# Kernel optimization log

Measured on AMD Instinct MI355X. Metric: run time of the kernel, lower is better.

The kernel has to match this reference:

```python
import jax, jax.numpy as jnp
import numpy as np

D_MODEL = 1024
N_HEADS = 16
HEAD_DIM = D_MODEL // N_HEADS


def setup_inputs() -> dict:
    key = jax.random.key(0)
    kx, kq, kk, kv, ko = jax.random.split(key, 5)
    B, S = 4, 2048
    scale = 0.02
    return {
        "x": jax.random.normal(kx, (B, S, D_MODEL), dtype=jnp.float32),
        "Wq": jax.random.normal(kq, (D_MODEL, D_MODEL), dtype=jnp.float32) * scale,
        "Wk": jax.random.normal(kk, (D_MODEL, HEAD_DIM), dtype=jnp.float32) * scale,
        "Wv": jax.random.normal(kv, (D_MODEL, HEAD_DIM), dtype=jnp.float32) * scale,
        "Wo": jax.random.normal(ko, (D_MODEL, D_MODEL), dtype=jnp.float32) * scale,
    }


def reference(x, Wq, Wk, Wv, Wo):
    B, S, _ = x.shape
    # Q: [B, H, S, hd]; K, V: [B, S, hd] shared across heads (MQA)
    Q = (x @ Wq).reshape(B, S, N_HEADS, HEAD_DIM).transpose(0, 2, 1, 3)
    K = x @ Wk
    V = x @ Wv
    # scores: [B, H, S, S]
    scores = jnp.einsum("bhqd,bkd->bhqk", Q, K) / jnp.sqrt(jnp.float32(HEAD_DIM))
    attn = jax.nn.softmax(scores, axis=-1)
    out = jnp.einsum("bhqk,bkd->bhqd", attn, V)  # [B, H, S, hd]
    out = out.transpose(0, 2, 1, 3).reshape(B, S, D_MODEL)
    return out @ Wo
```

## Files before the change

kernel.cpp:

```cpp
#include <hip/hip_runtime.h>
#include <hip/hip_bf16.h>

typedef __bf16  bf16x8  __attribute__((ext_vector_type(8)));
typedef __bf16  bf16x4  __attribute__((ext_vector_type(4)));
typedef float   f32x4   __attribute__((ext_vector_type(4)));
typedef unsigned short ushort8 __attribute__((ext_vector_type(8)));

#define D_MODEL 1024
#define HEAD_DIM 64
#define N_HEADS 16
#define BATCH 4
#define SEQ 2048
#define ROWS (BATCH*SEQ)
#define QKV_LD 1152
#define VT_LD 2080

#define AS1 __attribute__((address_space(1)))
#define AS3 __attribute__((address_space(3)))

static __device__ inline float exp2_fast(float x) {
  float r; asm("v_exp_f32 %0, %1" : "=v"(r) : "v"(x)); return r;
}

__global__ __launch_bounds__(256) void k_f32_to_bf16(const float* __restrict__ in,
                                                     __bf16* __restrict__ out, int n) {
  int i = (blockIdx.x * 256 + threadIdx.x) * 8;
  if (i >= n) return;
  float4 a = *(const float4*)(in + i);
  float4 b = *(const float4*)(in + i + 4);
  __bf16 r[8] __attribute__((aligned(16))) =
      {(__bf16)a.x,(__bf16)a.y,(__bf16)a.z,(__bf16)a.w,
       (__bf16)b.x,(__bf16)b.y,(__bf16)b.z,(__bf16)b.w};
  *(ushort8*)(out + i) = *(const ushort8*)r;
}

__global__ __launch_bounds__(256) void k_transpose_f32_bf16(const float* __restrict__ in,
                                                            __bf16* __restrict__ out,
                                                            int R, int C, float scale) {
  __shared__ float t[32][33];
  int tx = threadIdx.x & 31, ty = threadIdx.x >> 5;
  int r0 = blockIdx.y * 32, c0 = blockIdx.x * 32;
  #pragma unroll
  for (int i = 0; i < 4; ++i)
    t[ty + i*8][tx] = in[(size_t)(r0 + ty + i*8) * C + c0 + tx];
  __syncthreads();
  #pragma unroll
  for (int i = 0; i < 4; ++i)
    out[(size_t)(c0 + ty + i*8) * R + r0 + tx] = (__bf16)(t[tx][ty + i*8] * scale);
}

template<typename OUT_T>
__global__ __launch_bounds__(256) void k_gemm(const __bf16* __restrict__ A,
                                              const __bf16* __restrict__ Bt,
                                              OUT_T* __restrict__ C,
                                              int M, int N, int K) {
  __shared__ __bf16 As[2][128*32] __attribute__((aligned(16)));
  __shared__ __bf16 Bs[2][128*32] __attribute__((aligned(16)));
  const int tid  = threadIdx.x;
  const int lane = tid & 63, wave = tid >> 6;
  const int wm = wave >> 1, wn = wave & 1;
  const int l15 = lane & 15, lhi = lane >> 4;
  const int arow0 = blockIdx.x * 128;
  const int brow0 = blockIdx.y * 128;
  f32x4 acc[4][4] = {};
  const int srow = lane >> 2;
  const int scol = (lane & 3) * 8;
  const int nt = K >> 5;

  auto stage = [&](int t, int buf) {
    #pragma unroll
    for (int i = 0; i < 2; ++i) {
      int chunk = i*4 + wave;
      int r = chunk*16 + srow;
      __builtin_amdgcn_global_load_lds(
          (const AS1 unsigned int*)(A  + (size_t)(arow0 + r)*K + t*32 + scol),
          (AS3 unsigned int*)(&As[buf][0] + chunk*512), 16, 0, 0);
      __builtin_amdgcn_global_load_lds(
          (const AS1 unsigned int*)(Bt + (size_t)(brow0 + r)*K + t*32 + scol),
          (AS3 unsigned int*)(&Bs[buf][0] + chunk*512), 16, 0, 0);
    }
  };

  stage(0, 0);
  asm volatile("s_waitcnt vmcnt(0)" ::: "memory");
  __builtin_amdgcn_s_barrier();

  for (int t = 0; t < nt; ++t) {
    const int cur = t & 1;
    if (t + 1 < nt) stage(t + 1, cur ^ 1);
    bf16x8 af[4], bfr[4];
    #pragma unroll
    for (int m = 0; m < 4; ++m)
      af[m] = *(const bf16x8*)(&As[cur][0] + (wm*64 + m*16 + l15)*32 + lhi*8);
    #pragma unroll
    for (int n = 0; n < 4; ++n)
      bfr[n] = *(const bf16x8*)(&Bs[cur][0] + (wn*64 + n*16 + l15)*32 + lhi*8);
    #pragma unroll
    for (int m = 0; m < 4; ++m)
      #pragma unroll
      for (int n = 0; n < 4; ++n)
        acc[m][n] = __builtin_amdgcn_mfma_f32_16x16x32_bf16(af[m], bfr[n], acc[m][n], 0, 0, 0);
    asm volatile("s_waitcnt vmcnt(0)" ::: "memory");
    __builtin_amdgcn_s_barrier();
  }
  #pragma unroll
  for (int m = 0; m < 4; ++m)
    #pragma unroll
    for (int n = 0; n < 4; ++n) {
      int row = arow0 + wm*64 + m*16 + lhi*4;
      int col = brow0 + wn*64 + n*16 + l15;
      #pragma unroll
      for (int r = 0; r < 4; ++r)
        C[(size_t)(row + r) * N + col] = (OUT_T)acc[m][n][r];
    }
}

__global__ __launch_bounds__(256) void k_vt_split(const __bf16* __restrict__ QKV,
                                                  __bf16* __restrict__ Vt) {
  __shared__ __bf16 t[64][72] __attribute__((aligned(16)));
  int st = blockIdx.x, b = blockIdx.y;
  int tid = threadIdx.x;
  int rr = tid >> 3, cc = (tid & 7) * 8;
  #pragma unroll
  for (int i = 0; i < 2; ++i) {
    int s = rr + i*32;
    *(ushort8*)&t[s][cc] =
      *(const ushort8*)(QKV + (size_t)(b*SEQ + st*64 + s) * QKV_LD + 1088 + cc);
  }
  __syncthreads();
  #pragma unroll
  for (int i = 0; i < 2; ++i) {
    int d = rr + i*32;
    __bf16 tmp[8] __attribute__((aligned(16)));
    #pragma unroll
    for (int j = 0; j < 8; ++j) tmp[j] = t[cc + j][d];
    *(ushort8*)(Vt + (size_t)(b*64 + d) * VT_LD + st*64 + cc) = *(const ushort8*)tmp;
  }
}

__global__ __launch_bounds__(512, 4) void k_attn(const __bf16* __restrict__ QKV,
                                                 const __bf16* __restrict__ Vt,
                                                 __bf16* __restrict__ O) {
  __shared__ __bf16 Kl[2][64*64];
  __shared__ __bf16 Vl[2][64*64];
  __shared__ __bf16 Pl[8][32*64];
  const int qt = blockIdx.x, h = blockIdx.y, b = blockIdx.z;
  const int tid = threadIdx.x, lane = tid & 63, w = tid >> 6;
  const int l15 = lane & 15, lhi = lane >> 4;
  const int l7 = l15 & 7;

  const int srow = lane >> 3;
  const int j8   = lane & 7;
  const int row_t = w*8 + srow;
  const int jsrc = j8 ^ srow;
  const __bf16* Kg = QKV + (size_t)b*SEQ*QKV_LD + 1024;
  const __bf16* Vg = Vt  + (size_t)b*64*VT_LD;

  auto stage = [&](int t, int buf) {
    __builtin_amdgcn_global_load_lds(
        (const AS1 unsigned int*)(Kg + (size_t)(t*64 + row_t)*QKV_LD + jsrc*8),
        (AS3 unsigned int*)(&Kl[buf][0] + w*512), 16, 0, 0);
    __builtin_amdgcn_global_load_lds(
        (const AS1 unsigned int*)(Vg + (size_t)row_t*VT_LD + t*64 + jsrc*8),
        (AS3 unsigned int*)(&Vl[buf][0] + w*512), 16, 0, 0);
  };

  stage(0, 0);

  bf16x8 aq[2][2];
  {
    const __bf16* qp = QKV + (size_t)(b*SEQ + qt*256 + w*32 + l15)*QKV_LD + h*HEAD_DIM;
    aq[0][0] = *(const bf16x8*)(qp +               lhi*8);
    aq[0][1] = *(const bf16x8*)(qp +          32 + lhi*8);
    aq[1][0] = *(const bf16x8*)(qp + 16*QKV_LD +      lhi*8);
    aq[1][1] = *(const bf16x8*)(qp + 16*QKV_LD + 32 + lhi*8);
  }

  f32x4 oacc[2][4] = {};
  float mrun[2] = {-__builtin_inff(), -__builtin_inff()};
  float lrun[2] = {0.f, 0.f};

  asm volatile("s_waitcnt vmcnt(0)" ::: "memory");
  __builtin_amdgcn_s_barrier();

  for (int t = 0; t < SEQ/64; ++t) {
    const int cur = t & 1;
    if (t < SEQ/64 - 1) {
      stage(t+1, cur^1);
      asm volatile("s_waitcnt vmcnt(2)" ::: "memory");
    } else {
      asm volatile("s_waitcnt vmcnt(0)" ::: "memory");
    }
    const char* Kc = (const char*)&Kl[cur][0];
    const char* Vc = (const char*)&Vl[cur][0];

    f32x4 s[2][4] = {};
    __builtin_amdgcn_s_setprio(1);
    #pragma unroll
    for (int n = 0; n < 4; ++n) {
      const int key = n*16 + l15;
      bf16x8 kb0 = *(const bf16x8*)(Kc + key*128 + (((    lhi) ^ l7)*16));
      bf16x8 kb1 = *(const bf16x8*)(Kc + key*128 + (((4 + lhi) ^ l7)*16));
      #pragma unroll
      for (int m = 0; m < 2; ++m) {
        s[m][n] = __builtin_amdgcn_mfma_f32_16x16x32_bf16(kb0, aq[m][0], s[m][n], 0, 0, 0);
        s[m][n] = __builtin_amdgcn_mfma_f32_16x16x32_bf16(kb1, aq[m][1], s[m][n], 0, 0, 0);
      }
    }
    __builtin_amdgcn_s_setprio(0);

    float tm[2];
    #pragma unroll
    for (int m = 0; m < 2; ++m) {
      float a0 = fmaxf(fmaxf(s[m][0][0], s[m][0][1]), fmaxf(s[m][0][2], s[m][0][3]));
      float a1 = fmaxf(fmaxf(s[m][1][0], s[m][1][1]), fmaxf(s[m][1][2], s[m][1][3]));
      float a2 = fmaxf(fmaxf(s[m][2][0], s[m][2][1]), fmaxf(s[m][2][2], s[m][2][3]));
      float a3 = fmaxf(fmaxf(s[m][3][0], s[m][3][1]), fmaxf(s[m][3][2], s[m][3][3]));
      tm[m] = fmaxf(fmaxf(a0, a1), fmaxf(a2, a3));
      tm[m] = fmaxf(tm[m], __shfl_xor(tm[m], 16, 64));
      tm[m] = fmaxf(tm[m], __shfl_xor(tm[m], 32, 64));
    }

    int nogrow = (tm[0] <= mrun[0] + 8.f) && (tm[1] <= mrun[1] + 8.f);
    if (!__all(nogrow)) {
      float corr[2];
      #pragma unroll
      for (int m = 0; m < 2; ++m) {
        float mnew = fmaxf(mrun[m], tm[m]);
        corr[m] = exp2_fast(mrun[m] - mnew);
        mrun[m] = mnew;
        lrun[m] *= corr[m];
      }
      #pragma unroll
      for (int m = 0; m < 2; ++m) {
        float cb[4];
        #pragma unroll
        for (int r = 0; r < 4; ++r) cb[r] = __shfl(corr[m], lhi*4 + r, 64);
        #pragma unroll
        for (int n = 0; n < 4; ++n)
          #pragma unroll
          for (int r = 0; r < 4; ++r)
            oacc[m][n][r] *= cb[r];
      }
    }

    #pragma unroll
    for (int m = 0; m < 2; ++m) {
      const int prow = m*16 + l15;
      #pragma unroll
      for (int n = 0; n < 4; ++n) {
        bf16x4 pk;
        #pragma unroll
        for (int r = 0; r < 4; ++r) {
          float pv = exp2_fast(s[m][n][r] - mrun[m]);
          lrun[m] += pv;
          pk[r] = (__bf16)pv;
        }
        const int blk = (n*2 + (lhi>>1)) ^ l7;
        *(bf16x4*)((char*)&Pl[w][0] + prow*128 + blk*16 + (lhi&1)*8) = pk;
      }
    }

    bf16x8 ap0[2], ap1[2];
    #pragma unroll
    for (int m = 0; m < 2; ++m) {
      const char* pb = (const char*)&Pl[w][0] + (m*16 + l15)*128;
      ap0[m] = *(const bf16x8*)(pb + (((    lhi) ^ l7)*16));
      ap1[m] = *(const bf16x8*)(pb + (((4 + lhi) ^ l7)*16));
    }

    __builtin_amdgcn_s_setprio(1);
    #pragma unroll
    for (int n = 0; n < 4; ++n) {
      const int d = n*16 + l15;
      bf16x8 vb0 = *(const bf16x8*)(Vc + d*128 + (((    lhi) ^ l7)*16));
      bf16x8 vb1 = *(const bf16x8*)(Vc + d*128 + (((4 + lhi) ^ l7)*16));
      #pragma unroll
      for (int m = 0; m < 2; ++m) {
        oacc[m][n] = __builtin_amdgcn_mfma_f32_16x16x32_bf16(ap0[m], vb0, oacc[m][n], 0, 0, 0);
        oacc[m][n] = __builtin_amdgcn_mfma_f32_16x16x32_bf16(ap1[m], vb1, oacc[m][n], 0, 0, 0);
      }
    }
    __builtin_amdgcn_s_setprio(0);
    __builtin_amdgcn_s_barrier();
  }

  #pragma unroll
  for (int m = 0; m < 2; ++m) {
    lrun[m] += __shfl_xor(lrun[m], 16, 64);
    lrun[m] += __shfl_xor(lrun[m], 32, 64);
  }
  float rinv[2][4];
  #pragma unroll
  for (int m = 0; m < 2; ++m)
    #pragma unroll
    for (int r = 0; r < 4; ++r)
      rinv[m][r] = __builtin_amdgcn_rcpf(__shfl(lrun[m], lhi*4 + r, 64));
  #pragma unroll
  for (int m = 0; m < 2; ++m)
    #pragma unroll
    for (int n = 0; n < 4; ++n)
      #pragma unroll
      for (int r = 0; r < 4; ++r) {
        size_t row = (size_t)b*SEQ + qt*256 + w*32 + m*16 + lhi*4 + r;
        O[row * D_MODEL + h*HEAD_DIM + n*16 + l15] = (__bf16)(oacc[m][n][r] * rinv[m][r]);
      }
}

extern "C" void kernel_launch(void* const* d_in, const int* in_sizes, int n_in,
                              void* d_out, int out_size, void* d_ws, size_t ws_size,
                              hipStream_t stream) {
  const float* x  = (const float*)d_in[0];
  const float* Wq = (const float*)d_in[1];
  const float* Wk = (const float*)d_in[2];
  const float* Wv = (const float*)d_in[3];
  const float* Wo = (const float*)d_in[4];
  float* out = (float*)d_out;

  char* ws = (char*)d_ws;
  size_t off = 0;
  auto alloc = [&](size_t bytes) -> void* {
    void* p = ws + off;
    off += (bytes + 255) & ~(size_t)255;
    return p;
  };
  __bf16* xb    = (__bf16*)alloc((size_t)ROWS * D_MODEL * 2);
  __bf16* QKVb  = (__bf16*)alloc((size_t)ROWS * QKV_LD * 2);
  __bf16* WqkvT = (__bf16*)alloc((size_t)QKV_LD * D_MODEL * 2);
  __bf16* WoT   = (__bf16*)alloc((size_t)D_MODEL * D_MODEL * 2);
  __bf16* Vtb   = (__bf16*)alloc((size_t)BATCH * 64 * VT_LD * 2);

  const float SCALE_Q = 0.125f * 1.4426950408889634f;

  k_f32_to_bf16<<<ROWS*D_MODEL/2048, 256, 0, stream>>>(x, xb, ROWS*D_MODEL);
  k_transpose_f32_bf16<<<dim3(D_MODEL/32, D_MODEL/32), 256, 0, stream>>>(Wq, WqkvT, D_MODEL, D_MODEL, SCALE_Q);
  k_transpose_f32_bf16<<<dim3(HEAD_DIM/32, D_MODEL/32), 256, 0, stream>>>(Wk, WqkvT + (size_t)1024*D_MODEL, D_MODEL, HEAD_DIM, 1.0f);
  k_transpose_f32_bf16<<<dim3(HEAD_DIM/32, D_MODEL/32), 256, 0, stream>>>(Wv, WqkvT + (size_t)1088*D_MODEL, D_MODEL, HEAD_DIM, 1.0f);
  k_transpose_f32_bf16<<<dim3(D_MODEL/32, D_MODEL/32), 256, 0, stream>>>(Wo, WoT, D_MODEL, D_MODEL, 1.0f);

  k_gemm<__bf16><<<dim3(ROWS/128, QKV_LD/128), 256, 0, stream>>>(xb, WqkvT, QKVb, ROWS, QKV_LD, D_MODEL);
  k_vt_split<<<dim3(SEQ/64, BATCH), 256, 0, stream>>>(QKVb, Vtb);
  k_attn<<<dim3(SEQ/256, N_HEADS, BATCH), 512, 0, stream>>>(QKVb, Vtb, xb);
  k_gemm<float><<<dim3(ROWS/128, D_MODEL/128), 256, 0, stream>>>(xb, WoT, out, ROWS, D_MODEL, D_MODEL);
}
```

Before: 244.5 us.

## Keep softmax probabilities in registers by permuting V key order

Removes the per-warp LDS round trip for the P matrix in the attention kernel and feeds the exponentiated scores straight from registers into the PV MFMAs. To make the register layout of the QK accumulator line up with the A operand of the PV MFMA, the V-transpose kernel now writes keys in a permuted order within each 64-key tile. This saves LDS writes, reads and 32 KB of shared memory per block, which may raise occupancy. The risk is that the permutation must exactly match the MFMA output layout, or the results will be wrong.

```diff
diff --git a/kernel.cpp b/kernel.cpp
--- a/kernel.cpp
+++ b/kernel.cpp
@@ -133,7 +133,12 @@
     int d = rr + i*32;
     __bf16 tmp[8] __attribute__((aligned(16)));
     #pragma unroll
-    for (int j = 0; j < 8; ++j) tmp[j] = t[cc + j][d];
+    for (int jj = 0; jj < 8; ++jj) {
+      int pos = cc + jj;
+      int K = (pos & 3) | (((pos >> 3) & 1) << 2) | (((pos >> 4) & 1) << 3)
+            | (((pos >> 2) & 1) << 4) | (pos & 32);
+      tmp[jj] = t[K][d];
+    }
     *(ushort8*)(Vt + (size_t)(b*64 + d) * VT_LD + st*64 + cc) = *(const ushort8*)tmp;
   }
 }
@@ -143,7 +148,6 @@
                                                  __bf16* __restrict__ O) {
   __shared__ __bf16 Kl[2][64*64];
   __shared__ __bf16 Vl[2][64*64];
-  __shared__ __bf16 Pl[8][32*64];
   const int qt = blockIdx.x, h = blockIdx.y, b = blockIdx.z;
   const int tid = threadIdx.x, lane = tid & 63, w = tid >> 6;
   const int l15 = lane & 15, lhi = lane >> 4;
@@ -244,41 +248,28 @@
       }
     }
 
-    #pragma unroll
-    for (int m = 0; m < 2; ++m) {
-      const int prow = m*16 + l15;
-      #pragma unroll
-      for (int n = 0; n < 4; ++n) {
-        bf16x4 pk;
+    bf16x8 pa[2][2];
+    #pragma unroll
+    for (int m = 0; m < 2; ++m)
+      #pragma unroll
+      for (int n = 0; n < 4; ++n)
         #pragma unroll
         for (int r = 0; r < 4; ++r) {
           float pv = exp2_fast(s[m][n][r] - mrun[m]);
           lrun[m] += pv;
-          pk[r] = (__bf16)pv;
+          pa[m][n >> 1][(n & 1)*4 + r] = (__bf16)pv;
         }
-        const int blk = (n*2 + (lhi>>1)) ^ l7;
-        *(bf16x4*)((char*)&Pl[w][0] + prow*128 + blk*16 + (lhi&1)*8) = pk;
-      }
-    }
-
-    bf16x8 ap0[2], ap1[2];
-    #pragma unroll
-    for (int m = 0; m < 2; ++m) {
-      const char* pb = (const char*)&Pl[w][0] + (m*16 + l15)*128;
-      ap0[m] = *(const bf16x8*)(pb + (((    lhi) ^ l7)*16));
-      ap1[m] = *(const bf16x8*)(pb + (((4 + lhi) ^ l7)*16));
-    }
 
     __builtin_amdgcn_s_setprio(1);
     #pragma unroll
-    for (int n = 0; n < 4; ++n) {
-      const int d = n*16 + l15;
+    for (int dblk = 0; dblk < 4; ++dblk) {
+      const int d = dblk*16 + l15;
       bf16x8 vb0 = *(const bf16x8*)(Vc + d*128 + (((    lhi) ^ l7)*16));
       bf16x8 vb1 = *(const bf16x8*)(Vc + d*128 + (((4 + lhi) ^ l7)*16));
       #pragma unroll
       for (int m = 0; m < 2; ++m) {
-        oacc[m][n] = __builtin_amdgcn_mfma_f32_16x16x32_bf16(ap0[m], vb0, oacc[m][n], 0, 0, 0);
-        oacc[m][n] = __builtin_amdgcn_mfma_f32_16x16x32_bf16(ap1[m], vb1, oacc[m][n], 0, 0, 0);
+        oacc[m][dblk] = __builtin_amdgcn_mfma_f32_16x16x32_bf16(pa[m][0], vb0, oacc[m][dblk], 0, 0, 0);
+        oacc[m][dblk] = __builtin_amdgcn_mfma_f32_16x16x32_bf16(pa[m][1], vb1, oacc[m][dblk], 0, 0, 0);
       }
     }
     __builtin_amdgcn_s_setprio(0);
```

Result: faster. 239.1 us (-2.2%).
